# Performance work log

Measured on AMD Instinct MI355X. Metric: run time of the kernel, lower is better.

The kernel has to match this reference:

```python
import jax, jax.numpy as jnp
import numpy as np

B = 1 << 20
EMB = 8
N_BREEDS, N_TEMPS = 15, 9
HIDDENS = [128, 64, 32]
IN_DIM = (EMB * 2 + 9) * 2  # 50
EPS = 1e-5


def _encode_pet(breed, size, energy, temp, age, social, weight, breed_emb, temp_emb):
    # breed/temp: [B] int -> embedding gather [B,8]; size/energy -> one-hot [B,3]
    be = breed_emb[breed]
    te = temp_emb[temp]
    size_oh = jax.nn.one_hot(size, 3, dtype=be.dtype)
    energy_oh = jax.nn.one_hot(energy, 3, dtype=be.dtype)
    nums = jnp.stack([age / 15.0, social, weight / 100.0], axis=-1)  # [B,3]
    return jnp.concatenate([be, size_oh, energy_oh, te, nums], axis=-1)  # [B,25]


def _mlp(x, Ws, bs, gammas, betas, Wout, bout):
    for W, b, g, bt in zip(Ws, bs, gammas, betas):
        x = x @ W + b
        mu = jnp.mean(x, axis=0)
        var = jnp.mean(jnp.square(x - mu), axis=0)  # biased var (torch BN training)
        x = (x - mu) * jax.lax.rsqrt(var + EPS) * g + bt
        x = jax.nn.relu(x)
    x = x @ Wout + bout
    return jax.nn.sigmoid(x).squeeze(-1)  # [B]


def setup_inputs() -> dict:
    key = jax.random.key(0)
    ks = jax.random.split(key, 32)
    inp = {
        "pet1_breed": jax.random.randint(ks[0], (B,), 0, N_BREEDS, dtype=jnp.int32),
        "pet1_size": jax.random.randint(ks[1], (B,), 0, 3, dtype=jnp.int32),
        "pet1_energy": jax.random.randint(ks[2], (B,), 0, 3, dtype=jnp.int32),
        "pet1_temp": jax.random.randint(ks[3], (B,), 0, N_TEMPS, dtype=jnp.int32),
        "pet1_age": jax.random.uniform(ks[4], (B,)) * 15.0,
        "pet1_social": jax.random.uniform(ks[5], (B,)),
        "pet1_weight": jax.random.uniform(ks[6], (B,)) * 100.0,
        "pet2_breed": jax.random.randint(ks[7], (B,), 0, N_BREEDS, dtype=jnp.int32),
        "pet2_size": jax.random.randint(ks[8], (B,), 0, 3, dtype=jnp.int32),
        "pet2_energy": jax.random.randint(ks[9], (B,), 0, 3, dtype=jnp.int32),
        "pet2_temp": jax.random.randint(ks[10], (B,), 0, N_TEMPS, dtype=jnp.int32),
        "pet2_age": jax.random.uniform(ks[11], (B,)) * 15.0,
        "pet2_social": jax.random.uniform(ks[12], (B,)),
        "pet2_weight": jax.random.uniform(ks[13], (B,)) * 100.0,
        "breed_emb": jax.random.normal(ks[14], (N_BREEDS, EMB), dtype=jnp.float32),
        "temp_emb": jax.random.normal(ks[15], (N_TEMPS, EMB), dtype=jnp.float32),
    }
    prev = IN_DIM
    ki = 16
    for i, h in enumerate(HIDDENS, start=1):
        s = 1.0 / np.sqrt(prev)
        inp[f"W{i}"] = jax.random.uniform(ks[ki], (prev, h), minval=-s, maxval=s); ki += 1
        inp[f"b{i}"] = jax.random.uniform(ks[ki], (h,), minval=-s, maxval=s); ki += 1
        inp[f"gamma{i}"] = jnp.ones((h,), jnp.float32)
        inp[f"beta{i}"] = jnp.zeros((h,), jnp.float32)
        prev = h
    s = 1.0 / np.sqrt(prev)
    inp["W4"] = jax.random.uniform(ks[ki], (prev, 1), minval=-s, maxval=s); ki += 1
    inp["b4"] = jax.random.uniform(ks[ki], (1,), minval=-s, maxval=s)
    return inp


def reference(pet1_breed, pet1_size, pet1_energy, pet1_temp, pet1_age, pet1_social, pet1_weight,
              pet2_breed, pet2_size, pet2_energy, pet2_temp, pet2_age, pet2_social, pet2_weight,
              breed_emb, temp_emb,
              W1, b1, gamma1, beta1, W2, b2, gamma2, beta2, W3, b3, gamma3, beta3, W4, b4):
    f1 = _encode_pet(pet1_breed, pet1_size, pet1_energy, pet1_temp,
                     pet1_age, pet1_social, pet1_weight, breed_emb, temp_emb)
    f2 = _encode_pet(pet2_breed, pet2_size, pet2_energy, pet2_temp,
                     pet2_age, pet2_social, pet2_weight, breed_emb, temp_emb)
    x = jnp.concatenate([f1, f2], axis=-1)  # [B,50]
    return _mlp(x, [W1, W2, W3], [b1, b2, b3], [gamma1, gamma2, gamma3],
                [beta1, beta2, beta3], W4, b4)
```

## Files before the change

kernel.cpp:

```cpp
#include <hip/hip_runtime.h>
#include <hip/hip_bf16.h>

#define BATCH (1u<<20)
static constexpr float EPSBN = 1e-5f;
static constexpr float INV_B = 1.0f / (float)BATCH;

typedef unsigned int   uint;
typedef unsigned short ushort;

#define TSTR 132
#define NTABROWS 66
#define OFF_W2F    55296ULL
#define OFF_W3F    71680ULL
#define OFF_STATS  75776ULL
#define OFF_PARAMS 90112ULL
#define OFF_W1S    94208ULL
#define OFF_X2     147456ULL
#define OFF_X3D    (147456ULL + 134217728ULL)
#define T1_NEED    (147456ULL + 134217728ULL)
#define T2_NEED    (147456ULL + 134217728ULL + 67108864ULL)

struct Ptrs {
  const int *br1,*sz1,*en1,*tp1; const float *ag1,*so1,*wt1;
  const int *br2,*sz2,*en2,*tp2; const float *ag2,*so2,*wt2;
  const float *bemb,*temb;
  const float *W1,*b1,*g1,*be1;
  const float *W2,*b2,*g2,*be2;
  const float *W3,*b3,*g3,*be3;
  const float *W4,*b4;
  float* ws; float* out;
};

typedef __attribute__((ext_vector_type(8))) short bf16x8;
typedef __attribute__((ext_vector_type(4))) float f32x4;

__device__ __forceinline__ float4 ld4(const float* p) {
  return *reinterpret_cast<const float4*>(p);
}
__device__ __forceinline__ float4 f4add(float4 a, float4 b) {
  return make_float4(a.x+b.x, a.y+b.y, a.z+b.z, a.w+b.w);
}
__device__ __forceinline__ float4 f4fma(float4 a, float4 w, float s) {
  return make_float4(fmaf(w.x,s,a.x), fmaf(w.y,s,a.y), fmaf(w.z,s,a.z), fmaf(w.w,s,a.w));
}
__device__ __forceinline__ void add4(float4& a, const float4 b) {
  a.x += b.x; a.y += b.y; a.z += b.z; a.w += b.w;
}
__device__ __forceinline__ void fma4s(float4& a, const float4 b, float s) {
  a.x = fmaf(b.x, s, a.x); a.y = fmaf(b.y, s, a.y);
  a.z = fmaf(b.z, s, a.z); a.w = fmaf(b.w, s, a.w);
}

__device__ __forceinline__ ushort bfb(float f) {
  union { __hip_bfloat16 h; ushort u; } cv; cv.h = __float2bfloat16(f); return cv.u;
}
__device__ __forceinline__ uint pk2(float a, float b) {
  return ((uint)bfb(b) << 16) | (uint)bfb(a);
}
__device__ __forceinline__ uint pku(ushort a, ushort b) {
  return ((uint)b << 16) | (uint)a;
}
__device__ __forceinline__ bf16x8 ldfrag(const void* p) {
  union { uint4 u; bf16x8 v; } cv; cv.u = *reinterpret_cast<const uint4*>(p); return cv.v;
}
__device__ __forceinline__ bf16x8 mkfrag(uint a, uint b, uint c, uint d) {
  union { uint4 u; bf16x8 v; } cv; cv.u = make_uint4(a,b,c,d); return cv.v;
}
__device__ __forceinline__ float bflo(uint w) { return __uint_as_float(w << 16); }
__device__ __forceinline__ float bfhi(uint w) { return __uint_as_float(w & 0xffff0000u); }
__device__ __forceinline__ float bf2f(ushort u) { return __uint_as_float(((uint)u) << 16); }

struct SIdx { int r[8]; float v[6]; };
__device__ __forceinline__ SIdx load_idx(const Ptrs& P, unsigned s) {
  SIdx o;
  o.r[0] = P.br1[s];      o.r[1] = 15 + P.tp1[s];
  o.r[2] = 24 + P.br2[s]; o.r[3] = 39 + P.tp2[s];
  o.r[4] = 48 + P.sz1[s]; o.r[5] = 51 + P.en1[s];
  o.r[6] = 54 + P.sz2[s]; o.r[7] = 57 + P.en2[s];
  o.v[0] = P.ag1[s]*(1.0f/15.0f); o.v[1] = P.so1[s]; o.v[2] = P.wt1[s]*0.01f;
  o.v[3] = P.ag2[s]*(1.0f/15.0f); o.v[4] = P.so2[s]; o.v[5] = P.wt2[s]*0.01f;
  return o;
}

__device__ __forceinline__ float4 gather4(const float* Tl, const float* contT,
                                          const int rb[8], const float v[6], int c) {
  float4 A = f4add(f4add(ld4(Tl+rb[0]+c), ld4(Tl+rb[1]+c)),
                   f4add(ld4(Tl+rb[2]+c), ld4(Tl+rb[3]+c)));
  float4 B = f4add(f4add(ld4(Tl+rb[4]+c), ld4(Tl+rb[5]+c)),
                   f4add(ld4(Tl+rb[6]+c), ld4(Tl+rb[7]+c)));
  A = f4fma(A, ld4(contT + 60*TSTR + c), v[0]);
  A = f4fma(A, ld4(contT + 61*TSTR + c), v[1]);
  A = f4fma(A, ld4(contT + 62*TSTR + c), v[2]);
  B = f4fma(B, ld4(contT + 63*TSTR + c), v[3]);
  B = f4fma(B, ld4(contT + 64*TSTR + c), v[4]);
  B = f4fma(B, ld4(contT + 65*TSTR + c), v[5]);
  return f4add(A, B);
}

__device__ __forceinline__ void load_rb(const Ptrs& P, unsigned s, int rb[8], float v[6]) {
  SIdx o = load_idx(P, s);
  #pragma unroll
  for (int i = 0; i < 8; ++i) rb[i] = o.r[i]*TSTR;
  #pragma unroll
// ... 116 lines not shown
  else if (t < 12) { const int b = 4*(t-8)+q; return (b <= 14) ? 24 + b : -1; }
  else if (t < 15) { if (t == 14 && q >= 1) return 63 + (q-1); const int vv = 4*(t-12)+q; return (vv <= 8) ? 39 + vv : -1; }
  else if (t == 15){ return (q <= 2) ? 51 + q : -1; }
  else if (t == 16){ return (q <= 2) ? 54 + q : -1; }
  else if (t == 17){ return (q <= 2) ? 57 + q : -1; }
  return -1;
}


__global__ __launch_bounds__(256) void k_prep(Ptrs P) {
  const int t = threadIdx.x;
  float* T = P.ws;
  {
    float* st = (float*)((char*)P.ws + OFF_STATS);
    for (int i = t; i < 224*16; i += 256) st[i] = 0.0f;
  }
  if (t < 128) {
    const int c = t;
    for (int b = 0; b < 15; ++b) {
      float a1 = P.b1[c], a2 = 0.0f;
      #pragma unroll
      for (int e = 0; e < 8; ++e) {
        a1 = fmaf(P.bemb[b*8+e], P.W1[e*128 + c], a1);
        a2 = fmaf(P.bemb[b*8+e], P.W1[(25+e)*128 + c], a2);
      }
      T[b*TSTR + c] = a1; T[(24+b)*TSTR + c] = a2;
    }
    for (int tt = 0; tt < 9; ++tt) {
      float a1 = 0.0f, a2 = 0.0f;
      #pragma unroll
      for (int e = 0; e < 8; ++e) {
        a1 = fmaf(P.temb[tt*8+e], P.W1[(14+e)*128 + c], a1);
        a2 = fmaf(P.temb[tt*8+e], P.W1[(39+e)*128 + c], a2);
      }
      T[(15+tt)*TSTR + c] = a1; T[(39+tt)*TSTR + c] = a2;
    }
    #pragma unroll
    for (int i = 0; i < 3; ++i) {
      T[(48+i)*TSTR + c] = P.W1[(8+i)*128 + c];
      T[(51+i)*TSTR + c] = P.W1[(11+i)*128 + c];
      T[(54+i)*TSTR + c] = P.W1[(33+i)*128 + c];
      T[(57+i)*TSTR + c] = P.W1[(36+i)*128 + c];
    }
    const int cr[6] = {22,23,24,47,48,49};
    #pragma unroll
    for (int m = 0; m < 6; ++m) T[(60+m)*TSTR + c] = P.W1[cr[m]*128 + c];
  }
  __syncthreads();
  __hip_bfloat16* w2f = (__hip_bfloat16*)((char*)P.ws + OFF_W2F);
  for (int slot = t; slot < 1024; slot += 256) {
    const int fid = slot >> 6, l = slot & 63;
    const int mt = fid >> 2, kk = fid & 3, q = l >> 4, m = l & 15;
    #pragma unroll
    for (int e = 0; e < 8; ++e)
      w2f[slot*8 + e] = __float2bfloat16(P.W2[(kk*32 + 8*q + e)*64 + 16*mt + m]);
  }
  __hip_bfloat16* w3f = (__hip_bfloat16*)((char*)P.ws + OFF_W3F);
  for (int slot = t; slot < 256; slot += 256) {
    const int fid = slot >> 6, l = slot & 63;
    const int mt = fid >> 1, kk = fid & 1, q = l >> 4, m = l & 15;
    #pragma unroll
    for (int e = 0; e < 8; ++e)
      w3f[slot*8 + e] = __float2bfloat16(P.W3[(kk*32 + 8*q + e)*32 + 16*mt + m]);
  }
  uint4* w1s = (uint4*)((char*)P.ws + OFF_W1S);
  for (int slot = t; slot < 3072; slot += 256) {
    const int fid = slot >> 6, l = slot & 63;
    const int hl = fid & 1, mk = fid >> 1;
    const int kk = mk % 3, mt = mk / 3;
    const int q = l >> 4, m = l & 15, ch = 16*mt + m;
    ushort out[8];
    #pragma unroll
    for (int e = 0; e < 8; ++e) {
      const int row = frag_row(8*kk + e, q);
      const float val = (row >= 0) ? T[row*TSTR + ch] : 0.0f;
      const ushort hib = bfb(val);
      out[e] = (hl == 0) ? hib : bfb(val - bf2f(hib));
    }
    w1s[slot] = make_uint4(pku(out[0],out[1]), pku(out[2],out[3]),
                           pku(out[4],out[5]), pku(out[6],out[7]));
  }
}

__global__ __launch_bounds__(512) void k_stats1m(Ptrs P) {
  __shared__ __align__(16) char Wl[49152];
  __shared__ float sred[256];
  {
    const uint4* src = (const uint4*)((const char*)P.ws + OFF_W1S);
    uint4* dst = (uint4*)Wl;
    for (int i = threadIdx.x; i < 3072; i += 512) dst[i] = src[i];
  }
  if (threadIdx.x < 256) sred[threadIdx.x] = 0.f;
  __syncthreads();
  const int lane = threadIdx.x & 63;
  const int q = lane >> 4, m16 = lane & 15;
  const unsigned gw = (blockIdx.x*512 + threadIdx.x) >> 6;
  const unsigned nw = (gridDim.x*512) >> 6;
  const int mt0 = (gw & 1) * 4;
  const unsigned ts = nw >> 1;
  const unsigned NT = BATCH >> 4;
  f32x4 sums[4], sqs[4];
  #pragma unroll
  for (int mi = 0; mi < 4; ++mi) { sums[mi] = (f32x4){0,0,0,0}; sqs[mi] = (f32x4){0,0,0,0}; }
  const ushort ONE = 0x3F80;
  for (unsigned it = gw >> 1; it < NT; it += ts) {
    const unsigned s = it*16 + m16;
    const int c0 = P.br1[s], c1 = P.tp1[s], c2 = P.br2[s], c3 = P.tp2[s];
    const int c4i = P.sz1[s], c5 = P.en1[s], c6 = P.sz2[s], c7 = P.en2[s];
    const ushort vb0 = bfb(P.ag1[s]*(1.0f/15.0f)), vb1 = bfb(P.so1[s]);
    const ushort vb2 = bfb(P.wt1[s]*0.01f);
    const ushort vb3 = bfb(P.ag2[s]*(1.0f/15.0f)), vb4 = bfb(P.so2[s]);
    const ushort vb5 = bfb(P.wt2[s]*0.01f);
#define INDE(cv, tgt) ((ushort)(((cv) == (tgt)) ? ONE : 0))
    const ushort e0 = INDE(c0, q),     e1 = INDE(c0, 4+q);
    const ushort e2 = INDE(c0, 8+q);
    const ushort e3 = (q == 3) ? ONE : INDE(c0, 12+q);
    const ushort e4 = INDE(c1, q),     e5 = INDE(c1, 4+q);
    const ushort e6 = (q == 0) ? INDE(c1, 8)
                               : ((q == 1) ? vb0 : (q == 2) ? vb1 : vb2);
    const ushort e7 = INDE(c4i, q);
    const ushort f0 = INDE(c2, q),     f1 = INDE(c2, 4+q);
    const ushort f2 = INDE(c2, 8+q),   f3 = INDE(c2, 12+q);
    const ushort f4 = INDE(c3, q),     f5 = INDE(c3, 4+q);
    const ushort f6 = (q == 0) ? INDE(c3, 8)
                               : ((q == 1) ? vb3 : (q == 2) ? vb4 : vb5);
    const ushort f7 = INDE(c5, q);
    const ushort g0 = INDE(c6, q),     g1 = INDE(c7, q);
#undef INDE
    const bf16x8 B0 = mkfrag(pku(e0,e1), pku(e2,e3), pku(e4,e5), pku(e6,e7));
    const bf16x8 B1 = mkfrag(pku(f0,f1), pku(f2,f3), pku(f4,f5), pku(f6,f7));
    const bf16x8 B2 = mkfrag(pku(g0,g1), 0u, 0u, 0u);
    #pragma unroll
    for (int mi = 0; mi < 4; ++mi) {
      const int mt = mt0 + mi;
      f32x4 D = (f32x4){0.f,0.f,0.f,0.f};
      #pragma unroll
      for (int kk = 0; kk < 3; ++kk) {
        const bf16x8 bf = (kk == 0) ? B0 : (kk == 1) ? B1 : B2;
        const bf16x8 ah = ldfrag(Wl + (size_t)(((mt*3+kk)*2+0)*64 + lane)*16);
        D = __builtin_amdgcn_mfma_f32_16x16x32_bf16(ah, bf, D, 0, 0, 0);
        const bf16x8 al = ldfrag(Wl + (size_t)(((mt*3+kk)*2+1)*64 + lane)*16);
        D = __builtin_amdgcn_mfma_f32_16x16x32_bf16(al, bf, D, 0, 0, 0);
      }
      #pragma unroll
      for (int r = 0; r < 4; ++r) {
        sums[mi][r] += D[r];
        sqs[mi][r]   = fmaf(D[r], D[r], sqs[mi][r]);
      }
    }
  }
  #pragma unroll
  for (int d = 1; d <= 8; d <<= 1) {
    #pragma unroll
    for (int mi = 0; mi < 4; ++mi) {
      #pragma unroll
      for (int r = 0; r < 4; ++r) {
        sums[mi][r] += __shfl_xor(sums[mi][r], d, 64);
        sqs[mi][r]  += __shfl_xor(sqs[mi][r],  d, 64);
      }
    }
  }
  if (m16 == 0) {
    #pragma unroll
    for (int mi = 0; mi < 4; ++mi) {
      #pragma unroll
      for (int r = 0; r < 4; ++r) {
        const int ch = 16*(mt0 + mi) + 4*q + r;
        atomicAdd(&sred[ch], sums[mi][r]);
        atomicAdd(&sred[128+ch], sqs[mi][r]);
      }
    }
  }
  __syncthreads();
  if (threadIdx.x < 128) {
    float* stat = (float*)((char*)P.ws + OFF_STATS) + (size_t)threadIdx.x*16;
    atomicAdd(stat,     sred[threadIdx.x]);
    atomicAdd(stat + 8, sred[128+threadIdx.x]);
  }
}

__global__ __launch_bounds__(512) void k_stats1(Ptrs P) {
  __shared__ __align__(16) float Tl[60*TSTR];
  __shared__ float sred[256];
  for (int i = threadIdx.x; i < 60*TSTR; i += 512) Tl[i] = P.ws[i];
  if (threadIdx.x < 256) sred[threadIdx.x] = 0.f;
  __syncthreads();
  const int lane = threadIdx.x & 63;
  const int q = lane >> 4, m16 = lane & 15;
  const float* contT = P.ws;
  const unsigned gw = (blockIdx.x*512 + threadIdx.x) >> 6;
  const unsigned nw = (gridDim.x*512) >> 6;
  const int kk = gw & 3;
  const int c = kk*32 + 8*q;
  const unsigned NT = BATCH >> 4;
  unsigned it = gw >> 2;
  const unsigned ts = nw >> 2;
  float4 sa = make_float4(0,0,0,0), sb = sa, qa = sa, qb = sa;
  bool active = it < NT;
  int rb[8]; float v[6];
  if (active) load_rb(P, it*16 + m16, rb, v);
  while (active) {
    const unsigned itn = it + ts;
    const bool more = itn < NT;
    int rbn[8]; float vn[6];
    if (more) load_rb(P, itn*16 + m16, rbn, vn);
    const float4 xa = gather4(Tl, contT, rb, v, c);
    const float4 xb = gather4(Tl, contT, rb, v, c + 4);
    add4(sa, xa); add4(sb, xb);
    qa.x = fmaf(xa.x, xa.x, qa.x); qa.y = fmaf(xa.y, xa.y, qa.y);
    qa.z = fmaf(xa.z, xa.z, qa.z); qa.w = fmaf(xa.w, xa.w, qa.w);
    qb.x = fmaf(xb.x, xb.x, qb.x); qb.y = fmaf(xb.y, xb.y, qb.y);
    qb.z = fmaf(xb.z, xb.z, qb.z); qb.w = fmaf(xb.w, xb.w, qb.w);
    if (!more) break;
    #pragma unroll
    for (int i = 0; i < 8; ++i) rb[i] = rbn[i];
    #pragma unroll
    for (int i = 0; i < 6; ++i) v[i] = vn[i];
    it = itn;
  }
  #pragma unroll
  for (int d = 1; d <= 8; d <<= 1) {
    sa.x += __shfl_xor(sa.x, d, 64); sa.y += __shfl_xor(sa.y, d, 64);
    sa.z += __shfl_xor(sa.z, d, 64); sa.w += __shfl_xor(sa.w, d, 64);
    sb.x += __shfl_xor(sb.x, d, 64); sb.y += __shfl_xor(sb.y, d, 64);
    sb.z += __shfl_xor(sb.z, d, 64); sb.w += __shfl_xor(sb.w, d, 64);
    qa.x += __shfl_xor(qa.x, d, 64); qa.y += __shfl_xor(qa.y, d, 64);
    qa.z += __shfl_xor(qa.z, d, 64); qa.w += __shfl_xor(qa.w, d, 64);
    qb.x += __shfl_xor(qb.x, d, 64); qb.y += __shfl_xor(qb.y, d, 64);
    qb.z += __shfl_xor(qb.z, d, 64); qb.w += __shfl_xor(qb.w, d, 64);
  }
  if (m16 == 0) {
    atomicAdd(&sred[c+0], sa.x); atomicAdd(&sred[c+1], sa.y);
    atomicAdd(&sred[c+2], sa.z); atomicAdd(&sred[c+3], sa.w);
    atomicAdd(&sred[c+4], sb.x); atomicAdd(&sred[c+5], sb.y);
    atomicAdd(&sred[c+6], sb.z); atomicAdd(&sred[c+7], sb.w);
    atomicAdd(&sred[128+c+0], qa.x); atomicAdd(&sred[128+c+1], qa.y);
    atomicAdd(&sred[128+c+2], qa.z); atomicAdd(&sred[128+c+3], qa.w);
    atomicAdd(&sred[128+c+4], qb.x); atomicAdd(&sred[128+c+5], qb.y);
    atomicAdd(&sred[128+c+6], qb.z); atomicAdd(&sred[128+c+7], qb.w);
  }
  __syncthreads();
  if (threadIdx.x < 128) {
    float* stat = (float*)((char*)P.ws + OFF_STATS) + (size_t)threadIdx.x*16;
    atomicAdd(stat,     sred[threadIdx.x]);
    atomicAdd(stat + 8, sred[128+threadIdx.x]);
  }
}

__global__ void k_finalize(Ptrs P, int nch, int entry0, int pofs,
                           const float* g, const float* be) {
  const int c = threadIdx.x;
  if (c >= nch) return;
  const float* stat = (const float*)((const char*)P.ws + OFF_STATS) + (size_t)(entry0 + c)*16;
  const float mean = stat[0] * INV_B;
  const float var  = stat[8] * INV_B - mean*mean;
  const float inv  = 1.0f / sqrtf(var + EPSBN);
  const float scale = g[c] * inv;
  float* params = (float*)((char*)P.ws + OFF_PARAMS);
  params[pofs + c]       = scale;
  params[pofs + nch + c] = be[c] - mean * scale;
}

__global__ __launch_bounds__(512) void k_l2m(Ptrs P) {
  __shared__ __align__(16) float Tl[60*TSTR];
  __shared__ __align__(16) float bn[256];
  for (int i = threadIdx.x; i < 60*TSTR; i += 512) Tl[i] = P.ws[i];
  if (threadIdx.x < 128) {
    const float* stat = (const float*)((const char*)P.ws + OFF_STATS) + (size_t)threadIdx.x*16;
    const float mean = stat[0] * INV_B;
    const float var  = stat[8] * INV_B - mean*mean;
    const float scale = P.g1[threadIdx.x] / sqrtf(var + EPSBN);
    bn[threadIdx.x]       = scale;
    bn[128 + threadIdx.x] = P.be1[threadIdx.x] - mean * scale;
  }
  __syncthreads();
  const float* contT = P.ws;
  const int lane = threadIdx.x & 63;
  const int q = lane >> 4, m16 = lane & 15;
  const char* w2fB = (const char*)P.ws + OFF_W2F;
  char* x2B = (char*)P.ws + OFF_X2;
  const unsigned nw = (gridDim.x*512) >> 6;
  const unsigned NT = BATCH >> 4;
  unsigned it = (blockIdx.x*512 + threadIdx.x) >> 6;
  if (it >= NT) return;
  SIdx cur = load_idx(P, it*16 + m16);
  while (true) {
    const unsigned itn = it + nw;
    const bool more = itn < NT;
    SIdx nxt;
    if (more) nxt = load_idx(P, itn*16 + m16);
    const unsigned s = it*16 + m16;
    int rb[8];
    #pragma unroll
    for (int i = 0; i < 8; ++i) rb[i] = cur.r[i]*TSTR;
    f32x4 D[4];
    #pragma unroll
    for (int mt = 0; mt < 4; ++mt) {
      const float4 b = ld4(P.b2 + 16*mt + 4*q);
      D[mt][0] = b.x; D[mt][1] = b.y; D[mt][2] = b.z; D[mt][3] = b.w;
    }
    #pragma unroll
    for (int kk = 0; kk < 4; ++kk) {
      const int c = kk*32 + 8*q;
      const float4 xa = gather4(Tl, contT, rb, cur.v, c);
      const float4 xb = gather4(Tl, contT, rb, cur.v, c + 4);
      const float4 sca = ld4(bn + c), sha = ld4(bn + 128 + c);
      const float4 scb = ld4(bn + c + 4), shb = ld4(bn + 128 + c + 4);
      const float h0 = fmaxf(fmaf(xa.x, sca.x, sha.x), 0.f);
      const float h1 = fmaxf(fmaf(xa.y, sca.y, sha.y), 0.f);
      const float h2 = fmaxf(fmaf(xa.z, sca.z, sha.z), 0.f);
      const float h3 = fmaxf(fmaf(xa.w, sca.w, sha.w), 0.f);
      const float h4 = fmaxf(fmaf(xb.x, scb.x, shb.x), 0.f);
      const float h5 = fmaxf(fmaf(xb.y, scb.y, shb.y), 0.f);
      const float h6 = fmaxf(fmaf(xb.z, scb.z, shb.z), 0.f);
      const float h7 = fmaxf(fmaf(xb.w, scb.w, shb.w), 0.f);
      const bf16x8 bf = mkfrag(pk2(h0,h1), pk2(h2,h3), pk2(h4,h5), pk2(h6,h7));
      #pragma unroll
      for (int mt = 0; mt < 4; ++mt) {
        const bf16x8 af = ldfrag(w2fB + (size_t)((mt*4+kk)*64 + lane)*16);
        D[mt] = __builtin_amdgcn_mfma_f32_16x16x32_bf16(af, bf, D[mt], 0, 0, 0);
      }
    }
    #pragma unroll
    for (int mt = 0; mt < 4; ++mt) {
      const uint lo = pk2(D[mt][0], D[mt][1]);
      const uint hi = pk2(D[mt][2], D[mt][3]);
      *reinterpret_cast<uint2*>(x2B + (size_t)s*128 + (16*mt + 4*q)*2) = make_uint2(lo, hi);
    }
    if (!more) break;
    cur = nxt; it = itn;
  }
}

__global__ __launch_bounds__(256) void k_stats2(Ptrs P) {
  const uint* x2u = (const uint*)((const char*)P.ws + OFF_X2);
  const int pid = threadIdx.x & 31;
  const int lane = threadIdx.x & 63;
  const int w = threadIdx.x >> 6;
  float slo = 0.f, shi = 0.f, qlo = 0.f, qhi = 0.f;
  const unsigned r0 = blockIdx.x*8 + (threadIdx.x >> 5);
  const unsigned rs = gridDim.x*8;
  #pragma unroll 4
  for (unsigned r = r0; r < BATCH; r += rs) {
    const uint u = x2u[(size_t)r*32 + pid];
    const float lo = bflo(u), hi = bfhi(u);
    slo += lo; shi += hi;
    qlo = fmaf(lo, lo, qlo); qhi = fmaf(hi, hi, qhi);
  }
  slo += __shfl_xor(slo, 32, 64); shi += __shfl_xor(shi, 32, 64);
  qlo += __shfl_xor(qlo, 32, 64); qhi += __shfl_xor(qhi, 32, 64);
  __shared__ float red[512];
  if (lane < 32) {
    red[w*64 + 2*pid]       = slo; red[w*64 + 2*pid + 1]       = shi;
    red[256 + w*64 + 2*pid] = qlo; red[256 + w*64 + 2*pid + 1] = qhi;
  }
  __syncthreads();
  if (threadIdx.x < 64) {
    const int c = threadIdx.x;
    const float s  = red[c] + red[64+c] + red[128+c] + red[192+c];
    const float qq = red[256+c] + red[320+c] + red[384+c] + red[448+c];
    float* stat = (float*)((char*)P.ws + OFF_STATS) + (size_t)(128 + c)*16;
    atomicAdd(stat, s); atomicAdd(stat + 8, qq);
  }
}

__global__ __launch_bounds__(256) void k_l3m(Ptrs P, int dense) {
  __shared__ __align__(16) float bn[128];
  if (threadIdx.x < 64) {
    const float* stat = (const float*)((const char*)P.ws + OFF_STATS) + (size_t)(128 + threadIdx.x)*16;
    const float mean = stat[0] * INV_B;
    const float var  = stat[8] * INV_B - mean*mean;
    const float scale = P.g2[threadIdx.x] / sqrtf(var + EPSBN);
    bn[threadIdx.x]      = scale;
    bn[64 + threadIdx.x] = P.be2[threadIdx.x] - mean * scale;
  }
  __syncthreads();
  const int lane = threadIdx.x & 63;
  const int q = lane >> 4, m16 = lane & 15;
  const char* w3fB = (const char*)P.ws + OFF_W3F;
  const char* xB = (const char*)P.ws + OFF_X2;
  char* x3B = dense ? ((char*)P.ws + OFF_X3D) : ((char*)P.ws + OFF_X2);
  const size_t x3str = dense ? 64 : 128;
  const unsigned nw = (gridDim.x*256) >> 6;
  const unsigned NT = BATCH >> 4;
  unsigned it = (blockIdx.x*256 + threadIdx.x) >> 6;
  if (it >= NT) return;
  unsigned s = it*16 + m16;
  uint4 u0 = *reinterpret_cast<const uint4*>(xB + (size_t)s*128 + q*16);
  uint4 u1 = *reinterpret_cast<const uint4*>(xB + (size_t)s*128 + 64 + q*16);
  while (true) {
    const unsigned itn = it + nw;
    const bool more = itn < NT;
    uint4 n0, n1;
    if (more) {
      const unsigned sn = itn*16 + m16;
      n0 = *reinterpret_cast<const uint4*>(xB + (size_t)sn*128 + q*16);
      n1 = *reinterpret_cast<const uint4*>(xB + (size_t)sn*128 + 64 + q*16);
    }
    f32x4 D[2];
    #pragma unroll
    for (int mt = 0; mt < 2; ++mt) {
      const float4 b = ld4(P.b3 + 16*mt + 4*q);
      D[mt][0] = b.x; D[mt][1] = b.y; D[mt][2] = b.z; D[mt][3] = b.w;
    }
    #pragma unroll
    for (int kk = 0; kk < 2; ++kk) {
      const uint4 u = (kk == 0) ? u0 : u1;
      const int c = kk*32 + 8*q;
      const float4 scA = ld4(bn + c), shA = ld4(bn + 64 + c);
      const float4 scB = ld4(bn + c + 4), shB = ld4(bn + 64 + c + 4);
      const uint w[4] = {u.x,u.y,u.z,u.w};
      const float h0 = fmaxf(fmaf(bflo(w[0]), scA.x, shA.x), 0.f);
      const float h1 = fmaxf(fmaf(bfhi(w[0]), scA.y, shA.y), 0.f);
      const float h2 = fmaxf(fmaf(bflo(w[1]), scA.z, shA.z), 0.f);
      const float h3 = fmaxf(fmaf(bfhi(w[1]), scA.w, shA.w), 0.f);
      const float h4 = fmaxf(fmaf(bflo(w[2]), scB.x, shB.x), 0.f);
      const float h5 = fmaxf(fmaf(bfhi(w[2]), scB.y, shB.y), 0.f);
      const float h6 = fmaxf(fmaf(bflo(w[3]), scB.z, shB.z), 0.f);
      const float h7 = fmaxf(fmaf(bfhi(w[3]), scB.w, shB.w), 0.f);
      const bf16x8 bf = mkfrag(pk2(h0,h1), pk2(h2,h3), pk2(h4,h5), pk2(h6,h7));
      #pragma unroll
      for (int mt = 0; mt < 2; ++mt) {
        const bf16x8 af = ldfrag(w3fB + (size_t)((mt*2+kk)*64 + lane)*16);
        D[mt] = __builtin_amdgcn_mfma_f32_16x16x32_bf16(af, bf, D[mt], 0, 0, 0);
      }
    }
    #pragma unroll
    for (int mt = 0; mt < 2; ++mt) {
      const uint lo = pk2(D[mt][0], D[mt][1]);
      const uint hi = pk2(D[mt][2], D[mt][3]);
      *reinterpret_cast<uint2*>(x3B + (size_t)s*x3str + (16*mt + 4*q)*2) = make_uint2(lo, hi);
    }
    if (!more) break;
    u0 = n0; u1 = n1; it = itn; s = it*16 + m16;
  }
}

__global__ __launch_bounds__(256) void k_stats3(Ptrs P, int dense) {
  const uint* xu = dense ? (const uint*)((const char*)P.ws + OFF_X3D)
                         : (const uint*)((const char*)P.ws + OFF_X2);
  const unsigned rstr = dense ? 16 : 32;
  const int pid = threadIdx.x & 15;
  const int lane = threadIdx.x & 63;
  const int w = threadIdx.x >> 6;
  float slo = 0.f, shi = 0.f, qlo = 0.f, qhi = 0.f;
  const unsigned r0 = blockIdx.x*16 + (threadIdx.x >> 4);
  const unsigned rs = gridDim.x*16;
  #pragma unroll 4
  for (unsigned r = r0; r < BATCH; r += rs) {
    const uint u = xu[(size_t)r*rstr + pid];
    const float lo = bflo(u), hi = bfhi(u);
    slo += lo; shi += hi;
    qlo = fmaf(lo, lo, qlo); qhi = fmaf(hi, hi, qhi);
  }
  #pragma unroll
  for (int d = 16; d <= 32; d <<= 1) {
    slo += __shfl_xor(slo, d, 64); shi += __shfl_xor(shi, d, 64);
    qlo += __shfl_xor(qlo, d, 64); qhi += __shfl_xor(qhi, d, 64);
  }
  __shared__ float red[256];
  if (lane < 16) {
    red[w*32 + 2*pid]       = slo; red[w*32 + 2*pid + 1]       = shi;
    red[128 + w*32 + 2*pid] = qlo; red[128 + w*32 + 2*pid + 1] = qhi;
  }
  __syncthreads();
  if (threadIdx.x < 32) {
    const int c = threadIdx.x;
    const float s  = red[c] + red[32+c] + red[64+c] + red[96+c];
    const float qq = red[128+c] + red[160+c] + red[192+c] + red[224+c];
    float* stat = (float*)((char*)P.ws + OFF_STATS) + (size_t)(192 + c)*16;
    atomicAdd(stat, s); atomicAdd(stat + 8, qq);
  }
}

__global__ __launch_bounds__(256) void k_l4n(Ptrs P, int dense) {
  __shared__ float bn[64];
  if (threadIdx.x < 32) {
    const float* stat = (const float*)((const char*)P.ws + OFF_STATS) + (size_t)(192 + threadIdx.x)*16;
    const float mean = stat[0] * INV_B;
    const float var  = stat[8] * INV_B - mean*mean;
    const float scale = P.g3[threadIdx.x] / sqrtf(var + EPSBN);
    bn[threadIdx.x]      = scale;
    bn[32 + threadIdx.x] = P.be3[threadIdx.x] - mean * scale;
  }
  __syncthreads();
  const float* sc3 = bn, *sh3 = bn + 32;
  const char* xB = dense ? ((const char*)P.ws + OFF_X3D) : ((const char*)P.ws + OFF_X2);
  const size_t xstr = dense ? 64 : 128;
  const unsigned stride = gridDim.x * 256;
  for (unsigned s = blockIdx.x*256 + threadIdx.x; s < BATCH; s += stride) {
    float z = P.b4[0];
    #pragma unroll
    for (int c16 = 0; c16 < 4; ++c16) {
      const uint4 u = *reinterpret_cast<const uint4*>(xB + (size_t)s*xstr + c16*16);
      const uint w[4] = {u.x,u.y,u.z,u.w};
      #pragma unroll
      for (int j = 0; j < 4; ++j) {
        const int ch = c16*8 + 2*j;
        const float hlo = fmaxf(fmaf(bflo(w[j]), sc3[ch],   sh3[ch]),   0.f);
        const float hhi = fmaxf(fmaf(bfhi(w[j]), sc3[ch+1], sh3[ch+1]), 0.f);
        z = fmaf(hlo, P.W4[ch], z);
        z = fmaf(hhi, P.W4[ch+1], z);
      }
    }
    P.out[s] = 1.0f / (1.0f + __expf(-z));
  }
}

__global__ __launch_bounds__(256) void k_l2r(Ptrs P) {
  __shared__ __align__(16) float Tl[68*TSTR];
  __shared__ float red[512];
  const float* params = (const float*)((const char*)P.ws + OFF_PARAMS);
  stage_tab(P.ws, params, Tl, true);
  const int lane = threadIdx.x & 63;
  float4 sums[16], sqs[16];
  #pragma unroll
  for (int j4 = 0; j4 < 16; ++j4) {
    sums[j4] = make_float4(0.f,0.f,0.f,0.f);
    sqs[j4]  = make_float4(0.f,0.f,0.f,0.f);
  }
  const unsigned stride = gridDim.x * 256;
  for (unsigned s = blockIdx.x*256 + threadIdx.x; s < BATCH; s += stride) {
    int rb[8]; float v[6];
    load_rb(P, s, rb, v);
    float4 acc[16];
    x2_from_lds(Tl, rb, v, P.W2, P.b2, acc);
    #pragma unroll
    for (int j4 = 0; j4 < 16; ++j4) {
      add4(sums[j4], acc[j4]);
      sqs[j4].x = fmaf(acc[j4].x, acc[j4].x, sqs[j4].x);
      sqs[j4].y = fmaf(acc[j4].y, acc[j4].y, sqs[j4].y);
      sqs[j4].z = fmaf(acc[j4].z, acc[j4].z, sqs[j4].z);
      sqs[j4].w = fmaf(acc[j4].w, acc[j4].w, sqs[j4].w);
    }
  }
  const float psum = bfly64_from<false>(sums, lane);
  const float psq  = bfly64_from<false>(sqs,  lane);
  red[threadIdx.x] = psum; red[256 + threadIdx.x] = psq;
  __syncthreads();
  const int t = threadIdx.x;
  if (t < 64) {
    const float s0 = red[t] + red[t+64] + red[t+128] + red[t+192];
    const float q0 = red[256+t] + red[256+t+64] + red[256+t+128] + red[256+t+192];
    float* stat = (float*)((char*)P.ws + OFF_STATS) + (size_t)(128 + t)*16;
    atomicAdd(stat, s0); atomicAdd(stat + 8, q0);
  }
}

__global__ __launch_bounds__(256) void k_l3_rec(Ptrs P) {
  __shared__ __align__(16) float Tl[68*TSTR];
  __shared__ float red[512];
  const float* params = (const float*)((const char*)P.ws + OFF_PARAMS);
  stage_tab(P.ws, params, Tl, true);
  const float* sc2 = params + 256, *sh2 = params + 320;
  const int lane = threadIdx.x & 63;
  float4 sums3[8], sqs3[8];
  #pragma unroll
  for (int j4 = 0; j4 < 8; ++j4) {
    sums3[j4] = make_float4(0.f,0.f,0.f,0.f);
    sqs3[j4]  = make_float4(0.f,0.f,0.f,0.f);
  }
  const unsigned stride = gridDim.x * 256;
  for (unsigned s = blockIdx.x*256 + threadIdx.x; s < BATCH; s += stride) {
    int rb[8]; float v[6];
    load_rb(P, s, rb, v);
    float4 acc2[16];
    x2_from_lds(Tl, rb, v, P.W2, P.b2, acc2);
    float4 acc3[8];
    x3_from_acc2(acc2, P, sc2, sh2, acc3);
    #pragma unroll
    for (int j4 = 0; j4 < 8; ++j4) {
      add4(sums3[j4], acc3[j4]);
      sqs3[j4].x = fmaf(acc3[j4].x, acc3[j4].x, sqs3[j4].x);
      sqs3[j4].y = fmaf(acc3[j4].y, acc3[j4].y, sqs3[j4].y);
      sqs3[j4].z = fmaf(acc3[j4].z, acc3[j4].z, sqs3[j4].z);
      sqs3[j4].w = fmaf(acc3[j4].w, acc3[j4].w, sqs3[j4].w);
    }
  }
  const float psum = bfly32_from<false>(sums3, lane);
  const float psq  = bfly32_from<false>(sqs3,  lane);
  red[threadIdx.x] = psum; red[256 + threadIdx.x] = psq;
  __syncthreads();
  const int t = threadIdx.x;
  if (t < 32) {
    const float s0 = red[t] + red[t+64] + red[t+128] + red[t+192];
    const float q0 = red[256+t] + red[256+t+64] + red[256+t+128] + red[256+t+192];
    float* stat = (float*)((char*)P.ws + OFF_STATS) + (size_t)(192 + t)*16;
    atomicAdd(stat, s0); atomicAdd(stat + 8, q0);
  }
}

__global__ __launch_bounds__(256) void k_l4_rec(Ptrs P) {
  __shared__ __align__(16) float Tl[68*TSTR];
  const float* params = (const float*)((const char*)P.ws + OFF_PARAMS);
  stage_tab(P.ws, params, Tl, true);
  const float* sc2 = params + 256, *sh2 = params + 320;
  const float* sc3 = params + 384, *sh3 = params + 416;
  const unsigned stride = gridDim.x * 256;
  for (unsigned s = blockIdx.x*256 + threadIdx.x; s < BATCH; s += stride) {
    int rb[8]; float v[6];
    load_rb(P, s, rb, v);
    float4 acc2[16];
    x2_from_lds(Tl, rb, v, P.W2, P.b2, acc2);
    float4 acc3[8];
    x3_from_acc2(acc2, P, sc2, sh2, acc3);
    float z = P.b4[0];
    #pragma unroll
    for (int k4 = 0; k4 < 8; ++k4) {
      const float4 a = acc3[k4];
      const float4 sc = ld4(sc3 + k4*4), sh = ld4(sh3 + k4*4);
      z = fmaf(fmaxf(fmaf(a.x, sc.x, sh.x), 0.0f), P.W4[k4*4+0], z);
      z = fmaf(fmaxf(fmaf(a.y, sc.y, sh.y), 0.0f), P.W4[k4*4+1], z);
      z = fmaf(fmaxf(fmaf(a.z, sc.z, sh.z), 0.0f), P.W4[k4*4+2], z);
      z = fmaf(fmaxf(fmaf(a.w, sc.w, sh.w), 0.0f), P.W4[k4*4+3], z);
    }
    P.out[s] = 1.0f / (1.0f + __expf(-z));
  }
}


extern "C" void kernel_launch(void* const* d_in, const int* in_sizes, int n_in,
                              void* d_out, int out_size, void* d_ws, size_t ws_size,
                              hipStream_t stream) {
  Ptrs P;
  P.br1 = (const int*)d_in[0];  P.sz1 = (const int*)d_in[1];
  P.en1 = (const int*)d_in[2];  P.tp1 = (const int*)d_in[3];
  P.ag1 = (const float*)d_in[4]; P.so1 = (const float*)d_in[5]; P.wt1 = (const float*)d_in[6];
  P.br2 = (const int*)d_in[7];  P.sz2 = (const int*)d_in[8];
  P.en2 = (const int*)d_in[9];  P.tp2 = (const int*)d_in[10];
  P.ag2 = (const float*)d_in[11]; P.so2 = (const float*)d_in[12]; P.wt2 = (const float*)d_in[13];
  P.bemb = (const float*)d_in[14]; P.temb = (const float*)d_in[15];
  P.W1 = (const float*)d_in[16]; P.b1 = (const float*)d_in[17];
  P.g1 = (const float*)d_in[18]; P.be1 = (const float*)d_in[19];
  P.W2 = (const float*)d_in[20]; P.b2 = (const float*)d_in[21];
  P.g2 = (const float*)d_in[22]; P.be2 = (const float*)d_in[23];
  P.W3 = (const float*)d_in[24]; P.b3 = (const float*)d_in[25];
  P.g3 = (const float*)d_in[26]; P.be3 = (const float*)d_in[27];
  P.W4 = (const float*)d_in[28]; P.b4 = (const float*)d_in[29];
  P.ws = (float*)d_ws; P.out = (float*)d_out;

  const bool t1 = ws_size >= T1_NEED;
  const int dense = (ws_size >= T2_NEED) ? 1 : 0;

  hipLaunchKernelGGL(k_prep, dim3(1), dim3(256), 0, stream, P);
  if (t1) {
    hipLaunchKernelGGL(k_stats1m, dim3(1024), dim3(512), 0, stream, P);
    hipLaunchKernelGGL(k_l2m, dim3(1024), dim3(512), 0, stream, P);
    hipLaunchKernelGGL(k_stats2, dim3(1024), dim3(256), 0, stream, P);
    hipLaunchKernelGGL(k_l3m, dim3(2048), dim3(256), 0, stream, P, dense);
    hipLaunchKernelGGL(k_stats3, dim3(1024), dim3(256), 0, stream, P, dense);
    hipLaunchKernelGGL(k_l4n, dim3(2048), dim3(256), 0, stream, P, dense);
  } else {
    hipLaunchKernelGGL(k_stats1, dim3(1024), dim3(512), 0, stream, P);
    hipLaunchKernelGGL(k_finalize, dim3(1), dim3(128), 0, stream, P, 128, 0, 0, P.g1, P.be1);
    hipLaunchKernelGGL(k_l2r, dim3(1024), dim3(256), 0, stream, P);
    hipLaunchKernelGGL(k_finalize, dim3(1), dim3(64), 0, stream, P, 64, 128, 256, P.g2, P.be2);
    hipLaunchKernelGGL(k_l3_rec, dim3(1024), dim3(256), 0, stream, P);
    hipLaunchKernelGGL(k_finalize, dim3(1), dim3(32), 0, stream, P, 32, 192, 384, P.g3, P.be3);
    hipLaunchKernelGGL(k_l4_rec, dim3(2048), dim3(256), 0, stream, P);
  }
}
```

Baseline: 555.4 us.

## Materialize layer-1 pre-activations in stats pass and reuse them in layer 2

When the workspace is large enough, the layer-1 statistics kernel also writes the bf16 layer-1 outputs (256 B per sample) to a new X1 buffer. A new k_l2x kernel then streams this buffer instead of recomputing layer 1 from gathered embedding tables and raw inputs. This trades about 256 MB of extra write plus read traffic for skipping the layer-1 recomputation and input gathers. Buffer offsets for layer 3 are parameterized so the larger workspace tier can place X3 separately.

Result: no change. 557.9 us (+0.5%).

```diff
diff --git a/kernel.cpp b/kernel.cpp
--- a/kernel.cpp
+++ b/kernel.cpp
@@ -7,6 +7,7 @@
 
 typedef unsigned int   uint;
 typedef unsigned short ushort;
+typedef unsigned long long u64;
 
 #define TSTR 132
 #define NTABROWS 66
@@ -16,9 +17,11 @@
 #define OFF_PARAMS 90112ULL
 #define OFF_W1S    94208ULL
 #define OFF_X2     147456ULL
-#define OFF_X3D    (147456ULL + 134217728ULL)
+#define OFF_X1     (147456ULL + 134217728ULL)
+#define OFF_X3T3   (OFF_X1 + 268435456ULL)
 #define T1_NEED    (147456ULL + 134217728ULL)
-#define T2_NEED    (147456ULL + 134217728ULL + 67108864ULL)
+#define T2_NEED    (OFF_X1 + 67108864ULL)
+#define T3_NEED    (OFF_X3T3 + 67108864ULL)
 
 struct Ptrs {
   const int *br1,*sz1,*en1,*tp1; const float *ag1,*so1,*wt1;
@@ -301,7 +304,7 @@
   }
 }
 
-__global__ __launch_bounds__(512) void k_stats1m(Ptrs P) {
+__global__ __launch_bounds__(512) void k_stats1m(Ptrs P, int storex1) {
   __shared__ __align__(16) char Wl[49152];
   __shared__ float sred[256];
   {
@@ -318,6 +321,7 @@
   const int mt0 = (gw & 1) * 4;
   const unsigned ts = nw >> 1;
   const unsigned NT = BATCH >> 4;
+  char* x1B = (char*)P.ws + OFF_X1;
   f32x4 sums[4], sqs[4];
   #pragma unroll
   for (int mi = 0; mi < 4; ++mi) { sums[mi] = (f32x4){0,0,0,0}; sqs[mi] = (f32x4){0,0,0,0}; }
@@ -361,6 +365,11 @@
         const bf16x8 al = ldfrag(Wl + (size_t)(((mt*3+kk)*2+1)*64 + lane)*16);
         D = __builtin_amdgcn_mfma_f32_16x16x32_bf16(al, bf, D, 0, 0, 0);
       }
+      if (storex1) {
+        const uint lo = pk2(D[0], D[1]);
+        const uint hi = pk2(D[2], D[3]);
+        *reinterpret_cast<uint2*>(x1B + (size_t)s*256 + (16*mt + 4*q)*2) = make_uint2(lo, hi);
+      }
       #pragma unroll
       for (int r = 0; r < 4; ++r) {
         sums[mi][r] += D[r];
@@ -395,6 +404,152 @@
     float* stat = (float*)((char*)P.ws + OFF_STATS) + (size_t)threadIdx.x*16;
     atomicAdd(stat,     sred[threadIdx.x]);
     atomicAdd(stat + 8, sred[128+threadIdx.x]);
+  }
+}
+
+__global__ __launch_bounds__(256) void k_l2x(Ptrs P) {
+  __shared__ __align__(16) float bn[256];
+  if (threadIdx.x < 128) {
+    const float* stat = (const float*)((const char*)P.ws + OFF_STATS) + (size_t)threadIdx.x*16;
+    const float mean = stat[0] * INV_B;
+    const float var  = stat[8] * INV_B - mean*mean;
+    const float scale = P.g1[threadIdx.x] / sqrtf(var + EPSBN);
+    bn[threadIdx.x]       = scale;
+    bn[128 + threadIdx.x] = P.be1[threadIdx.x] - mean * scale;
+  }
+  __syncthreads();
+  const int lane = threadIdx.x & 63;
+  const int q = lane >> 4, m16 = lane & 15;
+  const char* w2fB = (const char*)P.ws + OFF_W2F;
+  const char* x1B = (const char*)P.ws + OFF_X1;
+  char* x2B = (char*)P.ws + OFF_X2;
+  const unsigned nw = (gridDim.x*256) >> 6;
+  const unsigned NT = BATCH >> 4;
+  unsigned it = (blockIdx.x*256 + threadIdx.x) >> 6;
+  if (it >= NT) return;
+  unsigned s = it*16 + m16;
+  uint4 x0 = *reinterpret_cast<const uint4*>(x1B + (size_t)s*256 +   0 + q*16);
+  uint4 x1 = *reinterpret_cast<const uint4*>(x1B + (size_t)s*256 +  64 + q*16);
+  uint4 x2 = *reinterpret_cast<const uint4*>(x1B + (size_t)s*256 + 128 + q*16);
+  uint4 x3 = *reinterpret_cast<const uint4*>(x1B + (size_t)s*256 + 192 + q*16);
+  while (true) {
+    const unsigned itn = it + nw;
+    const bool more = itn < NT;
+    uint4 n0, n1, n2, n3;
+    if (more) {
+      const size_t rb = (size_t)(itn*16 + m16)*256;
+      n0 = *reinterpret_cast<const uint4*>(x1B + rb +   0 + q*16);
+      n1 = *reinterpret_cast<const uint4*>(x1B + rb +  64 + q*16);
+      n2 = *reinterpret_cast<const uint4*>(x1B + rb + 128 + q*16);
+      n3 = *reinterpret_cast<const uint4*>(x1B + rb + 192 + q*16);
+    }
+    f32x4 D[4];
+    #pragma unroll
+    for (int mt = 0; mt < 4; ++mt) {
+      const float4 b = ld4(P.b2 + 16*mt + 4*q);
+      D[mt][0] = b.x; D[mt][1] = b.y; D[mt][2] = b.z; D[mt][3] = b.w;
+    }
+    #pragma unroll
+    for (int kk = 0; kk < 4; ++kk) {
+      const uint4 u = (kk == 0) ? x0 : (kk == 1) ? x1 : (kk == 2) ? x2 : x3;
+      const int c = kk*32 + 8*q;
+      const float4 scA = ld4(bn + c), shA = ld4(bn + 128 + c);
+      const float4 scB = ld4(bn + c + 4), shB = ld4(bn + 128 + c + 4);
+      const uint w[4] = {u.x,u.y,u.z,u.w};
+      const float h0 = fmaxf(fmaf(bflo(w[0]), scA.x, shA.x), 0.f);
+      const float h1 = fmaxf(fmaf(bfhi(w[0]), scA.y, shA.y), 0.f);
+      const float h2 = fmaxf(fmaf(bflo(w[1]), scA.z, shA.z), 0.f);
+      const float h3 = fmaxf(fmaf(bfhi(w[1]), scA.w, shA.w), 0.f);
+      const float h4 = fmaxf(fmaf(bflo(w[2]), scB.x, shB.x), 0.f);
+      const float h5 = fmaxf(fmaf(bfhi(w[2]), scB.y, shB.y), 0.f);
+      const float h6 = fmaxf(fmaf(bflo(w[3]), scB.z, shB.z), 0.f);
+      const float h7 = fmaxf(fmaf(bfhi(w[3]), scB.w, shB.w), 0.f);
+      const bf16x8 bf = mkfrag(pk2(h0,h1), pk2(h2,h3), pk2(h4,h5), pk2(h6,h7));
+      #pragma unroll
+      for (int mt = 0; mt < 4; ++mt) {
+        const bf16x8 af = ldfrag(w2fB + (size_t)((mt*4+kk)*64 + lane)*16);
+        D[mt] = __builtin_amdgcn_mfma_f32_16x16x32_bf16(af, bf, D[mt], 0, 0, 0);
+      }
+    }
+    #pragma unroll
+    for (int mt = 0; mt < 4; ++mt) {
+      const uint lo = pk2(D[mt][0], D[mt][1]);
+      const uint hi = pk2(D[mt][2], D[mt][3]);
+      *reinterpret_cast<uint2*>(x2B + (size_t)s*128 + (16*mt + 4*q)*2) = make_uint2(lo, hi);
+    }
+    if (!more) break;
+    x0 = n0; x1 = n1; x2 = n2; x3 = n3; it = itn; s = it*16 + m16;
+  }
+}
+
+__global__ __launch_bounds__(512) void k_l2m(Ptrs P) {
+  __shared__ __align__(16) float Tl[60*TSTR];
+  __shared__ __align__(16) float bn[256];
+  for (int i = threadIdx.x; i < 60*TSTR; i += 512) Tl[i] = P.ws[i];
+  if (threadIdx.x < 128) {
+    const float* stat = (const float*)((const char*)P.ws + OFF_STATS) + (size_t)threadIdx.x*16;
+    const float mean = stat[0] * INV_B;
+    const float var  = stat[8] * INV_B - mean*mean;
+    const float scale = P.g1[threadIdx.x] / sqrtf(var + EPSBN);
+    bn[threadIdx.x]       = scale;
+    bn[128 + threadIdx.x] = P.be1[threadIdx.x] - mean * scale;
+  }
+  __syncthreads();
+  const float* contT = P.ws;
+  const int lane = threadIdx.x & 63;
+  const int q = lane >> 4, m16 = lane & 15;
+  const char* w2fB = (const char*)P.ws + OFF_W2F;
+  char* x2B = (char*)P.ws + OFF_X2;
+  const unsigned nw = (gridDim.x*512) >> 6;
+  const unsigned NT = BATCH >> 4;
+  unsigned it = (blockIdx.x*512 + threadIdx.x) >> 6;
+  if (it >= NT) return;
+  SIdx cur = load_idx(P, it*16 + m16);
+  while (true) {
+    const unsigned itn = it + nw;
+    const bool more = itn < NT;
+    SIdx nxt;
+    if (more) nxt = load_idx(P, itn*16 + m16);
+    const unsigned s = it*16 + m16;
+    int rb[8];
+    #pragma unroll
+    for (int i = 0; i < 8; ++i) rb[i] = cur.r[i]*TSTR;
+    f32x4 D[4];
+    #pragma unroll
+    for (int mt = 0; mt < 4; ++mt) {
+      const float4 b = ld4(P.b2 + 16*mt + 4*q);
+      D[mt][0] = b.x; D[mt][1] = b.y; D[mt][2] = b.z; D[mt][3] = b.w;
+    }
+    #pragma unroll
+    for (int kk = 0; kk < 4; ++kk) {
+      const int c = kk*32 + 8*q;
+      const float4 xa = gather4(Tl, contT, rb, cur.v, c);
+      const float4 xb = gather4(Tl, contT, rb, cur.v, c + 4);
+      const float4 sca = ld4(bn + c), sha = ld4(bn + 128 + c);
+      const float4 scb = ld4(bn + c + 4), shb = ld4(bn + 128 + c + 4);
+      const float h0 = fmaxf(fmaf(xa.x, sca.x, sha.x), 0.f);
+      const float h1 = fmaxf(fmaf(xa.y, sca.y, sha.y), 0.f);
+      const float h2 = fmaxf(fmaf(xa.z, sca.z, sha.z), 0.f);
+      const float h3 = fmaxf(fmaf(xa.w, sca.w, sha.w), 0.f);
+      const float h4 = fmaxf(fmaf(xb.x, scb.x, shb.x), 0.f);
+      const float h5 = fmaxf(fmaf(xb.y, scb.y, shb.y), 0.f);
+      const float h6 = fmaxf(fmaf(xb.z, scb.z, shb.z), 0.f);
+      const float h7 = fmaxf(fmaf(xb.w, scb.w, shb.w), 0.f);
+      const bf16x8 bf = mkfrag(pk2(h0,h1), pk2(h2,h3), pk2(h4,h5), pk2(h6,h7));
+      #pragma unroll
+      for (int mt = 0; mt < 4; ++mt) {
+        const bf16x8 af = ldfrag(w2fB + (size_t)((mt*4+kk)*64 + lane)*16);
+        D[mt] = __builtin_amdgcn_mfma_f32_16x16x32_bf16(af, bf, D[mt], 0, 0, 0);
+      }
+    }
+    #pragma unroll
+    for (int mt = 0; mt < 4; ++mt) {
+      const uint lo = pk2(D[mt][0], D[mt][1]);
+      const uint hi = pk2(D[mt][2], D[mt][3]);
+      *reinterpret_cast<uint2*>(x2B + (size_t)s*128 + (16*mt + 4*q)*2) = make_uint2(lo, hi);
+    }
+    if (!more) break;
+    cur = nxt; it = itn;
   }
 }
 
@@ -480,77 +635,6 @@
   params[pofs + nch + c] = be[c] - mean * scale;
 }
 
-__global__ __launch_bounds__(512) void k_l2m(Ptrs P) {
-  __shared__ __align__(16) float Tl[60*TSTR];
-  __shared__ __align__(16) float bn[256];
-  for (int i = threadIdx.x; i < 60*TSTR; i += 512) Tl[i] = P.ws[i];
-  if (threadIdx.x < 128) {
-    const float* stat = (const float*)((const char*)P.ws + OFF_STATS) + (size_t)threadIdx.x*16;
-    const float mean = stat[0] * INV_B;
-    const float var  = stat[8] * INV_B - mean*mean;
-    const float scale = P.g1[threadIdx.x] / sqrtf(var + EPSBN);
-    bn[threadIdx.x]       = scale;
-    bn[128 + threadIdx.x] = P.be1[threadIdx.x] - mean * scale;
-  }
-  __syncthreads();
-  const float* contT = P.ws;
-  const int lane = threadIdx.x & 63;
-  const int q = lane >> 4, m16 = lane & 15;
-  const char* w2fB = (const char*)P.ws + OFF_W2F;
-  char* x2B = (char*)P.ws + OFF_X2;
-  const unsigned nw = (gridDim.x*512) >> 6;
-  const unsigned NT = BATCH >> 4;
-  unsigned it = (blockIdx.x*512 + threadIdx.x) >> 6;
-  if (it >= NT) return;
-  SIdx cur = load_idx(P, it*16 + m16);
-  while (true) {
-    const unsigned itn = it + nw;
-    const bool more = itn < NT;
-    SIdx nxt;
-    if (more) nxt = load_idx(P, itn*16 + m16);
-    const unsigned s = it*16 + m16;
-    int rb[8];
-    #pragma unroll
-    for (int i = 0; i < 8; ++i) rb[i] = cur.r[i]*TSTR;
-    f32x4 D[4];
-    #pragma unroll
-    for (int mt = 0; mt < 4; ++mt) {
-      const float4 b = ld4(P.b2 + 16*mt + 4*q);
-      D[mt][0] = b.x; D[mt][1] = b.y; D[mt][2] = b.z; D[mt][3] = b.w;
-    }
-    #pragma unroll
-    for (int kk = 0; kk < 4; ++kk) {
-      const int c = kk*32 + 8*q;
-      const float4 xa = gather4(Tl, contT, rb, cur.v, c);
-      const float4 xb = gather4(Tl, contT, rb, cur.v, c + 4);
-      const float4 sca = ld4(bn + c), sha = ld4(bn + 128 + c);
-      const float4 scb = ld4(bn + c + 4), shb = ld4(bn + 128 + c + 4);
-      const float h0 = fmaxf(fmaf(xa.x, sca.x, sha.x), 0.f);
-      const float h1 = fmaxf(fmaf(xa.y, sca.y, sha.y), 0.f);
-      const float h2 = fmaxf(fmaf(xa.z, sca.z, sha.z), 0.f);
-      const float h3 = fmaxf(fmaf(xa.w, sca.w, sha.w), 0.f);
-      const float h4 = fmaxf(fmaf(xb.x, scb.x, shb.x), 0.f);
-      const float h5 = fmaxf(fmaf(xb.y, scb.y, shb.y), 0.f);
-      const float h6 = fmaxf(fmaf(xb.z, scb.z, shb.z), 0.f);
-      const float h7 = fmaxf(fmaf(xb.w, scb.w, shb.w), 0.f);
-      const bf16x8 bf = mkfrag(pk2(h0,h1), pk2(h2,h3), pk2(h4,h5), pk2(h6,h7));
-      #pragma unroll
-      for (int mt = 0; mt < 4; ++mt) {
-        const bf16x8 af = ldfrag(w2fB + (size_t)((mt*4+kk)*64 + lane)*16);
-        D[mt] = __builtin_amdgcn_mfma_f32_16x16x32_bf16(af, bf, D[mt], 0, 0, 0);
-      }
-    }
-    #pragma unroll
-    for (int mt = 0; mt < 4; ++mt) {
-      const uint lo = pk2(D[mt][0], D[mt][1]);
-      const uint hi = pk2(D[mt][2], D[mt][3]);
-      *reinterpret_cast<uint2*>(x2B + (size_t)s*128 + (16*mt + 4*q)*2) = make_uint2(lo, hi);
-    }
-    if (!more) break;
-    cur = nxt; it = itn;
-  }
-}
-
 __global__ __launch_bounds__(256) void k_stats2(Ptrs P) {
   const uint* x2u = (const uint*)((const char*)P.ws + OFF_X2);
   const int pid = threadIdx.x & 31;
@@ -583,7 +667,7 @@
   }
 }
 
-__global__ __launch_bounds__(256) void k_l3m(Ptrs P, int dense) {
+__global__ __launch_bounds__(256) void k_l3m(Ptrs P, u64 x3off, int x3str) {
   __shared__ __align__(16) float bn[128];
   if (threadIdx.x < 64) {
     const float* stat = (const float*)((const char*)P.ws + OFF_STATS) + (size_t)(128 + threadIdx.x)*16;
@@ -598,8 +682,7 @@
   const int q = lane >> 4, m16 = lane & 15;
   const char* w3fB = (const char*)P.ws + OFF_W3F;
   const char* xB = (const char*)P.ws + OFF_X2;
-  char* x3B = dense ? ((char*)P.ws + OFF_X3D) : ((char*)P.ws + OFF_X2);
-  const size_t x3str = dense ? 64 : 128;
+  char* x3B = (char*)P.ws + x3off;
   const unsigned nw = (gridDim.x*256) >> 6;
   const unsigned NT = BATCH >> 4;
   unsigned it = (blockIdx.x*256 + threadIdx.x) >> 6;
@@ -655,10 +738,8 @@
   }
 }
 
-__global__ __launch_bounds__(256) void k_stats3(Ptrs P, int dense) {
-  const uint* xu = dense ? (const uint*)((const char*)P.ws + OFF_X3D)
-                         : (const uint*)((const char*)P.ws + OFF_X2);
-  const unsigned rstr = dense ? 16 : 32;
+__global__ __launch_bounds__(256) void k_stats3(Ptrs P, u64 x3off, int rstrU) {
+  const uint* xu = (const uint*)((const char*)P.ws + x3off);
   const int pid = threadIdx.x & 15;
   const int lane = threadIdx.x & 63;
   const int w = threadIdx.x >> 6;
@@ -667,7 +748,7 @@
   const unsigned rs = gridDim.x*16;
   #pragma unroll 4
   for (unsigned r = r0; r < BATCH; r += rs) {
-    const uint u = xu[(size_t)r*rstr + pid];
+    const uint u = xu[(size_t)r*rstrU + pid];
     const float lo = bflo(u), hi = bfhi(u);
     slo += lo; shi += hi;
     qlo = fmaf(lo, lo, qlo); qhi = fmaf(hi, hi, qhi);
@@ -692,7 +773,7 @@
   }
 }
 
-__global__ __launch_bounds__(256) void k_l4n(Ptrs P, int dense) {
+__global__ __launch_bounds__(256) void k_l4n(Ptrs P, u64 x3off, int x3str) {
   __shared__ float bn[64];
   if (threadIdx.x < 32) {
     const float* stat = (const float*)((const char*)P.ws + OFF_STATS) + (size_t)(192 + threadIdx.x)*16;
@@ -704,14 +785,13 @@
   }
   __syncthreads();
   const float* sc3 = bn, *sh3 = bn + 32;
-  const char* xB = dense ? ((const char*)P.ws + OFF_X3D) : ((const char*)P.ws + OFF_X2);
-  const size_t xstr = dense ? 64 : 128;
+  const char* xB = (const char*)P.ws + x3off;
   const unsigned stride = gridDim.x * 256;
   for (unsigned s = blockIdx.x*256 + threadIdx.x; s < BATCH; s += stride) {
     float z = P.b4[0];
     #pragma unroll
     for (int c16 = 0; c16 < 4; ++c16) {
-      const uint4 u = *reinterpret_cast<const uint4*>(xB + (size_t)s*xstr + c16*16);
+      const uint4 u = *reinterpret_cast<const uint4*>(xB + (size_t)s*x3str + c16*16);
       const uint w[4] = {u.x,u.y,u.z,u.w};
       #pragma unroll
       for (int j = 0; j < 4; ++j) {
@@ -859,16 +939,28 @@
   P.ws = (float*)d_ws; P.out = (float*)d_out;
 
   const bool t1 = ws_size >= T1_NEED;
-  const int dense = (ws_size >= T2_NEED) ? 1 : 0;
+  const bool t2 = ws_size >= T2_NEED;
+  const bool t3 = ws_size >= T3_NEED;
+  u64 x3off; int x3str;
+  if (t3)      { x3off = OFF_X3T3; x3str = 64; }
+  else if (t2) { x3off = OFF_X1;   x3str = 64; }
+  else         { x3off = OFF_X2;   x3str = 128; }
 
   hipLaunchKernelGGL(k_prep, dim3(1), dim3(256), 0, stream, P);
-  if (t1) {
-    hipLaunchKernelGGL(k_stats1m, dim3(1024), dim3(512), 0, stream, P);
+  if (t3) {
+    hipLaunchKernelGGL(k_stats1m, dim3(1024), dim3(512), 0, stream, P, 1);
+    hipLaunchKernelGGL(k_l2x, dim3(2048), dim3(256), 0, stream, P);
+    hipLaunchKernelGGL(k_stats2, dim3(1024), dim3(256), 0, stream, P);
+    hipLaunchKernelGGL(k_l3m, dim3(2048), dim3(256), 0, stream, P, x3off, x3str);
+    hipLaunchKernelGGL(k_stats3, dim3(1024), dim3(256), 0, stream, P, x3off, x3str/4);
+    hipLaunchKernelGGL(k_l4n, dim3(2048), dim3(256), 0, stream, P, x3off, x3str);
+  } else if (t1) {
+    hipLaunchKernelGGL(k_stats1m, dim3(1024), dim3(512), 0, stream, P, 0);
     hipLaunchKernelGGL(k_l2m, dim3(1024), dim3(512), 0, stream, P);
     hipLaunchKernelGGL(k_stats2, dim3(1024), dim3(256), 0, stream, P);
-    hipLaunchKernelGGL(k_l3m, dim3(2048), dim3(256), 0, stream, P, dense);
-    hipLaunchKernelGGL(k_stats3, dim3(1024), dim3(256), 0, stream, P, dense);
-    hipLaunchKernelGGL(k_l4n, dim3(2048), dim3(256), 0, stream, P, dense);
+    hipLaunchKernelGGL(k_l3m, dim3(2048), dim3(256), 0, stream, P, x3off, x3str);
+    hipLaunchKernelGGL(k_stats3, dim3(1024), dim3(256), 0, stream, P, x3off, x3str/4);
+    hipLaunchKernelGGL(k_l4n, dim3(2048), dim3(256), 0, stream, P, x3off, x3str);
   } else {
     hipLaunchKernelGGL(k_stats1, dim3(1024), dim3(512), 0, stream, P);
     hipLaunchKernelGGL(k_finalize, dim3(1), dim3(128), 0, stream, P, 128, 0, 0, P.g1, P.be1);
```
